# Performance work log

Measured on AMD Instinct MI355X. Metric: run time of the kernel, lower is better.

The kernel has to match this reference:

```python
import jax, jax.numpy as jnp
import numpy as np

N = 50000
E = 800000
D_IN = 128
H = 128
K = 64
BN_EPS = 1e-5


def setup_inputs() -> dict:
    key = jax.random.key(0)
    ks = jax.random.split(key, 16)
    s_in = 1.0 / np.sqrt(D_IN)
    s_h = 1.0 / np.sqrt(H)
    inp = {
        "x": jax.random.normal(ks[0], (N, D_IN), dtype=jnp.float32),
        "edge_index": jax.random.randint(ks[1], (2, E), 0, N, dtype=jnp.int64),
        # GIN layer 1 MLP (Linear(D_IN,H) -> ReLU -> Linear(H,H)), eps1, BN1
        "W1a": jax.random.uniform(ks[2], (D_IN, H), jnp.float32, -s_in, s_in),
        "b1a": jnp.zeros((H,), jnp.float32),
        "W1b": jax.random.uniform(ks[3], (H, H), jnp.float32, -s_h, s_h),
        "b1b": jnp.zeros((H,), jnp.float32),
        "eps1": jnp.zeros((), jnp.float32),
        "gamma1": jnp.ones((H,), jnp.float32),
        "beta1": jnp.zeros((H,), jnp.float32),
        # GIN layer 2 MLP, eps2, BN2
        "W2a": jax.random.uniform(ks[4], (H, H), jnp.float32, -s_h, s_h),
        "b2a": jnp.zeros((H,), jnp.float32),
        "W2b": jax.random.uniform(ks[5], (H, H), jnp.float32, -s_h, s_h),
        "b2b": jnp.zeros((H,), jnp.float32),
        "eps2": jnp.zeros((), jnp.float32),
        "gamma2": jnp.ones((H,), jnp.float32),
        "beta2": jnp.zeros((H,), jnp.float32),
        # final projection (no bias) and learnable log temperature
        "Wout": jax.random.uniform(ks[6], (H, K), jnp.float32, -s_h, s_h),
        "log_tau": jnp.zeros((), jnp.float32),  # log(1.0)
    }
    return inp


def _gin_layer(x, src, dst, Wa, ba, Wb, bb, eps):
    # GINConv: mlp((1+eps)*x + sum_{j in N(i)} x_j), scatter-add over edges
    agg = jax.ops.segment_sum(x[src], dst, num_segments=N)  # [N, d]
    h = (1.0 + eps) * x + agg
    h = jax.nn.relu(h @ Wa + ba) @ Wb + bb
    return h


def _batchnorm(x, gamma, beta):
    # training-mode BatchNorm1d over node dim (biased variance)
    m = jnp.mean(x, axis=0)
    v = jnp.mean(jnp.square(x - m), axis=0)
    return (x - m) * jax.lax.rsqrt(v + BN_EPS) * gamma + beta


def reference(x, edge_index, W1a, b1a, W1b, b1b, eps1, gamma1, beta1,
              W2a, b2a, W2b, b2b, eps2, gamma2, beta2, Wout, log_tau):
    src, dst = edge_index[0], edge_index[1]
    h = _gin_layer(x, src, dst, W1a, b1a, W1b, b1b, eps1)
    h = jax.nn.relu(_batchnorm(h, gamma1, beta1))
    h = _gin_layer(h, src, dst, W2a, b2a, W2b, b2b, eps2)
    h = jax.nn.relu(_batchnorm(h, gamma2, beta2))
    logits = h @ Wout  # [N, K]
    tau = jnp.exp(log_tau)
    S = jax.nn.softmax(logits / tau, axis=-1)
    return (S, logits)
```

## Files before the change

### kernel.cpp

```cpp
#include <hip/hip_runtime.h>
#include <hip/hip_fp16.h>


#define NNODES 50000
#define NEDGES 800000
#define HD 128
#define KOUT 64
#define NCLS 8
#define CLSW 6250
#define HIST_BLKS 512

typedef __attribute__((ext_vector_type(8))) _Float16 f16x8;
typedef __attribute__((ext_vector_type(4))) float f32x4;

__device__ __forceinline__ unsigned short f2h_bits(float f) {
    _Float16 h = (_Float16)f;
    return __builtin_bit_cast(unsigned short, h);
}
__device__ __forceinline__ f16x8 h8_relu(f16x8 v) {
    #pragma unroll
    for (int i = 0; i < 8; ++i) v[i] = (v[i] > (_Float16)0.f) ? v[i] : (_Float16)0.f;
    return v;
}

__global__ __launch_bounds__(256) void prep_all(
    const float* __restrict__ x, unsigned short* __restrict__ xh,
    const float* __restrict__ W1a, const float* __restrict__ W1b,
    const float* __restrict__ W2a, const float* __restrict__ W2b,
    unsigned short* __restrict__ wt1a, unsigned short* __restrict__ wt1b,
    unsigned short* __restrict__ wt2a, unsigned short* __restrict__ wt2b,
    const int* __restrict__ ei, int* __restrict__ deg)
{
    __shared__ int h[CLSW];
    int bid = blockIdx.x;
    if (bid < HIST_BLKS) {
        const int cls = bid & 7;
        const int lo = cls * CLSW;
        const int e0 = (bid >> 3) * 12500;
        for (int i = threadIdx.x; i < CLSW; i += 256) h[i] = 0;
        __syncthreads();
        for (int e = e0 + threadIdx.x; e < e0 + 12500; e += 256) {
            unsigned d = (unsigned)(ei[NEDGES + e] - lo);
            if (d < (unsigned)CLSW) atomicAdd(&h[d], 1);
        }
        __syncthreads();
        for (int i = threadIdx.x; i < CLSW; i += 256) {
            int v = h[i];
            if (v) atomicAdd(&deg[lo + i], v);
        }
    } else if (bid < HIST_BLKS + 6250) {
        int i = (bid - HIST_BLKS) * 256 + threadIdx.x;
        float4 v = ((const float4*)x)[i];
        ushort4 o;
        o.x = f2h_bits(v.x); o.y = f2h_bits(v.y);
        o.z = f2h_bits(v.z); o.w = f2h_bits(v.w);
        ((ushort4*)xh)[i] = o;
    } else {
        int wb = bid - (HIST_BLKS + 6250);
        int w = wb >> 6;
        int idx = (wb & 63) * 256 + threadIdx.x;
        int n = idx >> 7, k = idx & 127;
        const float* W = (w == 0) ? W1a : (w == 1) ? W1b : (w == 2) ? W2a : W2b;
        unsigned short* Wt = (w == 0) ? wt1a : (w == 1) ? wt1b : (w == 2) ? wt2a : wt2b;
        Wt[idx] = f2h_bits(W[k * HD + n]);
    }
}

__global__ __launch_bounds__(256) void scan_a(
    const int* __restrict__ deg, int* __restrict__ incl, int* __restrict__ bsum)
{
    __shared__ int s[256];
    int t = threadIdx.x, idx = blockIdx.x * 256 + t;
    int v = (idx < NNODES) ? deg[idx] : 0;
    s[t] = v; __syncthreads();
    #pragma unroll
    for (int off = 1; off < 256; off <<= 1) {
        int tmp = (t >= off) ? s[t - off] : 0;
        __syncthreads();
        s[t] += tmp;
        __syncthreads();
    }
    if (idx < NNODES) incl[idx] = s[t];
    if (t == 255) bsum[blockIdx.x] = s[255];
}

__global__ __launch_bounds__(256) void scan_b(
    const int* __restrict__ bsum, int* __restrict__ bscan, int nblk)
{
    __shared__ int s[256];
    int t = threadIdx.x;
    s[t] = (t < nblk) ? bsum[t] : 0; __syncthreads();
    #pragma unroll
    for (int off = 1; off < 256; off <<= 1) {
        int tmp = (t >= off) ? s[t - off] : 0;
        __syncthreads();
        s[t] += tmp;
        __syncthreads();
    }
    bscan[t] = s[t];
}

__global__ __launch_bounds__(256) void scan_c(
    const int* __restrict__ deg, const int* __restrict__ incl,
    const int* __restrict__ bscan,
    int* __restrict__ row_start, int* __restrict__ cur)
{
    int b = blockIdx.x, t = threadIdx.x, idx = b * 256 + t;
    if (idx >= NNODES) return;
    int off = (b > 0) ? bscan[b - 1] : 0;
    int ex = incl[idx] - deg[idx] + off;
    row_start[idx] = ex;
    cur[idx] = ex;
}

__global__ __launch_bounds__(256) void edge_fill(
    const int* __restrict__ ei, int* __restrict__ cur, int* __restrict__ col)
{
    const int cls = blockIdx.x & 7;
    const int e0 = (blockIdx.x >> 3) * 3125;
    for (int e = e0 + threadIdx.x; e < e0 + 3125; e += 256) {
        int dst = ei[NEDGES + e];
        if (dst / CLSW == cls) {
            int pos = atomicAdd(&cur[dst], 1);
            col[pos] = ei[e];
        }
    }
}

template<bool BN>
__global__ __launch_bounds__(256) void gin_gather_w(
    const unsigned short* __restrict__ Xh, const int* __restrict__ col,
    const int* __restrict__ rs, const int* __restrict__ re,
    const float* __restrict__ eps,
    const float* __restrict__ ssum, const float* __restrict__ ssq,
    const float* __restrict__ gamma, const float* __restrict__ beta,
    unsigned short* __restrict__ H0h)
{
    __shared__ float s_sc[128], s_sh[128];
    const int t = threadIdx.x;
    const int g = t >> 4;
    const int lane = t & 15;
    const f16x8* X8 = (const f16x8*)Xh;
    const float alphaf = 1.f + eps[0];

    if (BN) {
        if (t < 128) {
            const float invN = 1.0f / (float)NNODES;
            float m = ssum[t] * invN;
            float var = fmaf(-m, m, ssq[t] * invN);
            float rsq = rsqrtf(var + 1e-5f);
            float sc = gamma[t] * rsq;
            s_sc[t] = sc;
            s_sh[t] = fmaf(-m, sc, beta[t]);
        }
        __syncthreads();
    }

    f16x8 sc8, sh8, al8;
    #pragma unroll
    for (int i = 0; i < 8; ++i) al8[i] = (_Float16)alphaf;
    if (BN) {
        #pragma unroll
        for (int i = 0; i < 8; ++i) {
            sc8[i] = (_Float16)s_sc[lane * 8 + i];
            sh8[i] = (_Float16)s_sh[lane * 8 + i];
        }
    }

    #pragma unroll 1
    for (int nn = 0; nn < 2; ++nn) {
        int node = blockIdx.x * 32 + nn * 16 + g;
        if (node >= NNODES) continue;

        f16x8 acc = X8[(long)node * 16 + lane];
        if (BN) acc = h8_relu(acc * sc8 + sh8);
        acc = acc * al8;

        int j = rs[node], end = re[node];
        for (; j + 3 < end; j += 4) {
            f16x8 u0 = X8[(long)col[j]     * 16 + lane];
            f16x8 u1 = X8[(long)col[j + 1] * 16 + lane];
            f16x8 u2 = X8[(long)col[j + 2] * 16 + lane];
            f16x8 u3 = X8[(long)col[j + 3] * 16 + lane];
            if (BN) {
                u0 = h8_relu(u0 * sc8 + sh8);
                u1 = h8_relu(u1 * sc8 + sh8);
                u2 = h8_relu(u2 * sc8 + sh8);
                u3 = h8_relu(u3 * sc8 + sh8);
            }
            acc += (u0 + u1) + (u2 + u3);
        }
        for (; j < end; ++j) {
            f16x8 u = X8[(long)col[j] * 16 + lane];
            if (BN) u = h8_relu(u * sc8 + sh8);
            acc += u;
        }

        ((f16x8*)H0h)[(long)node * 16 + lane] = acc;
    }
}

__global__ __launch_bounds__(256) void mlp_mfma(
    const unsigned short* __restrict__ A,
    const unsigned short* __restrict__ Wta,
    const float* __restrict__ biasa,
    const unsigned short* __restrict__ Wtb,
    const float* __restrict__ biasb,
    unsigned short* __restrict__ Cb,
    float* __restrict__ Cf,
    float* __restrict__ out_sum, float* __restrict__ out_sq)
{
    __shared__ float4 smem4[(34816 + 17408) / 16];
    char* smem = (char*)smem4;
    _Float16 (*Wbuf)[136] = (_Float16(*)[136])smem;
    _Float16 (*Cs16)[136] = (_Float16(*)[136])(smem + 34816);
    float (*CsF)[132] = (float(*)[132])smem;
    float* redp = (float*)(smem + 34816);

    const int t = threadIdx.x;
    const int wave = t >> 6, lane = t & 63;
    const int m16 = lane & 15, quad = lane >> 4;
    const int row0 = blockIdx.x * 64;
    const int arow = row0 + wave * 16 + m16;

    float4 wreg[8];
    #pragma unroll
    for (int i = 0; i < 8; ++i) {
        int idx = t + i * 256;
        int r = idx >> 4, s = idx & 15;
        *(float4*)&Wbuf[r][s * 8] = ((const float4*)Wta)[idx];
        wreg[i] = ((const float4*)Wtb)[idx];
    }

    f16x8 afrag[4];
    if (arow < NNODES) {
        const _Float16* ar = (const _Float16*)A + (long)arow * HD + quad * 8;
        #pragma unroll
        for (int kc = 0; kc < 4; ++kc)
            afrag[kc] = *(const f16x8*)(ar + kc * 32);
    } else {
        #pragma unroll
        for (int kc = 0; kc < 4; ++kc)
            afrag[kc] = f16x8{0, 0, 0, 0, 0, 0, 0, 0};
    }
    __syncthreads();

    f32x4 accs[8];
    #pragma unroll
    for (int np = 0; np < 8; np += 2) {
        f32x4 a0 = {0.f, 0.f, 0.f, 0.f};
        f32x4 a1 = {0.f, 0.f, 0.f, 0.f};
        const _Float16* b0 = &Wbuf[np * 16 + m16][quad * 8];
        const _Float16* b1 = &Wbuf[(np + 1) * 16 + m16][quad * 8];
        #pragma unroll
        for (int kc = 0; kc < 4; ++kc) {
            f16x8 f0 = *(const f16x8*)(b0 + kc * 32);
            f16x8 f1 = *(const f16x8*)(b1 + kc * 32);
            a0 = __builtin_amdgcn_mfma_f32_16x16x32_f16(afrag[kc], f0, a0, 0, 0, 0);
            a1 = __builtin_amdgcn_mfma_f32_16x16x32_f16(afrag[kc], f1, a1, 0, 0, 0);
        }
        accs[np] = a0; accs[np + 1] = a1;
    }
    __syncthreads();

    #pragma unroll
    for (int i = 0; i < 8; ++i) {
        int idx = t + i * 256;
        int r = idx >> 4, s = idx & 15;
        *(float4*)&Wbuf[r][s * 8] = wreg[i];
    }
    #pragma unroll
    for (int np = 0; np < 8; ++np) {
        int c = np * 16 + m16;
        float bb = biasa[c];
        #pragma unroll
        for (int r = 0; r < 4; ++r)
            Cs16[wave * 16 + quad * 4 + r][c] =
                (_Float16)fmaxf(accs[np][r] + bb, 0.f);
    }
    __syncthreads();

    f16x8 afrag2[4];
    {
        const int crow = wave * 16 + m16;
        #pragma unroll
        for (int kc = 0; kc < 4; ++kc)
            afrag2[kc] = *(const f16x8*)&Cs16[crow][quad * 8 + kc * 32];
    }
    #pragma unroll
    for (int np = 0; np < 8; np += 2) {
        f32x4 a0 = {0.f, 0.f, 0.f, 0.f};
        f32x4 a1 = {0.f, 0.f, 0.f, 0.f};
        const _Float16* b0 = &Wbuf[np * 16 + m16][quad * 8];
        const _Float16* b1 = &Wbuf[(np + 1) * 16 + m16][quad * 8];
        #pragma unroll
        for (int kc = 0; kc < 4; ++kc) {
            f16x8 f0 = *(const f16x8*)(b0 + kc * 32);
            f16x8 f1 = *(const f16x8*)(b1 + kc * 32);
            a0 = __builtin_amdgcn_mfma_f32_16x16x32_f16(afrag2[kc], f0, a0, 0, 0, 0);
            a1 = __builtin_amdgcn_mfma_f32_16x16x32_f16(afrag2[kc], f1, a1, 0, 0, 0);
        }
        accs[np] = a0; accs[np + 1] = a1;
    }
    __syncthreads();

    #pragma unroll
    for (int np = 0; np < 8; ++np) {
        int c = np * 16 + m16;
        float bb = biasb[c];
        #pragma unroll
        for (int r = 0; r < 4; ++r)
            CsF[wave * 16 + quad * 4 + r][c] = accs[np][r] + bb;
    }
    __syncthreads();

    const int s4 = t & 31;
    const int rb = t >> 5;
    float lsum[4] = {}, lsq[4] = {};
    #pragma unroll
    for (int i = 0; i < 8; ++i) {
        int r = rb + i * 8;
        int row = row0 + r;
        float4 v = *(const float4*)&CsF[r][s4 * 4];
        if (row < NNODES) {
            if (Cb) {
                ushort4 o;
                o.x = f2h_bits(v.x); o.y = f2h_bits(v.y);
                o.z = f2h_bits(v.z); o.w = f2h_bits(v.w);
                ((ushort4*)Cb)[(long)row * 32 + s4] = o;
            }
            if (Cf) ((float4*)Cf)[(long)row * 32 + s4] = v;
            lsum[0] += v.x; lsum[1] += v.y; lsum[2] += v.z; lsum[3] += v.w;
            lsq[0] = fmaf(v.x, v.x, lsq[0]);
            lsq[1] = fmaf(v.y, v.y, lsq[1]);
            lsq[2] = fmaf(v.z, v.z, lsq[2]);
            lsq[3] = fmaf(v.w, v.w, lsq[3]);
        }
    }
    #pragma unroll
    for (int j = 0; j < 4; ++j) {
        redp[(0 * 8 + rb) * 128 + s4 * 4 + j] = lsum[j];
        redp[(1 * 8 + rb) * 128 + s4 * 4 + j] = lsq[j];
    }
    __syncthreads();
    if (t < 128) {
        float s = 0.f, q = 0.f;
        #pragma unroll
        for (int g = 0; g < 8; ++g) {
            s += redp[g * 128 + t];
            q += redp[(8 + g) * 128 + t];
        }
        atomicAdd(&out_sum[t], s);
        atomicAdd(&out_sq[t],  q);
    }
}

__global__ __launch_bounds__(256) void out_proj_softmax(
    const float* __restrict__ H, const float* __restrict__ Wout,
    const float* __restrict__ ssum, const float* __restrict__ ssq,
    const float* __restrict__ gamma, const float* __restrict__ beta,
    const float* __restrict__ log_tau,
    float* __restrict__ outS, float* __restrict__ outL)
{
    __shared__ float As[HD][20];
    __shared__ float s_sc[128], s_sh[128];
    const int t = threadIdx.x;
    const long row0 = (long)blockIdx.x * 16;

    if (t < 128) {
        const float invN = 1.0f / (float)NNODES;
        float m = ssum[t] * invN;
        float var = fmaf(-m, m, ssq[t] * invN);
        float rsq = rsqrtf(var + 1e-5f);
        float sc = gamma[t] * rsq;
        s_sc[t] = sc;
        s_sh[t] = fmaf(-m, sc, beta[t]);
    }
    __syncthreads();

    #pragma unroll
    for (int i = 0; i < 8; ++i) {
        int idx = t + i * 256;
        int r = idx >> 7, cc = idx & 127;
        float v = H[(row0 + r) * HD + cc];
        As[cc][r] = fmaxf(fmaf(v, s_sc[cc], s_sh[cc]), 0.f);
    }
    __syncthreads();

    const int c = t & 63;
    const int g = t >> 6;
    float acc[4] = {};

    float wq[8];
    #pragma unroll
    for (int i = 0; i < 8; ++i) wq[i] = Wout[i * KOUT + c];

    #pragma unroll 1
    for (int kc = 0; kc < HD; kc += 8) {
        float wn[8];
        if (kc + 8 < HD) {
            #pragma unroll
            for (int i = 0; i < 8; ++i) wn[i] = Wout[(kc + 8 + i) * KOUT + c];
        }
        #pragma unroll
        for (int i = 0; i < 8; ++i) {
            float4 a = *(const float4*)&As[kc + i][g * 4];
            acc[0] = fmaf(a.x, wq[i], acc[0]);
            acc[1] = fmaf(a.y, wq[i], acc[1]);
            acc[2] = fmaf(a.z, wq[i], acc[2]);
            acc[3] = fmaf(a.w, wq[i], acc[3]);
        }
        if (kc + 8 < HD) {
            #pragma unroll
            for (int i = 0; i < 8; ++i) wq[i] = wn[i];
        }
    }

    float inv_tau = __expf(-log_tau[0]);
    #pragma unroll
    for (int i = 0; i < 4; ++i) {
        float z = acc[i] * inv_tau;
        float m = z;
        #pragma unroll
        for (int o = 32; o > 0; o >>= 1) m = fmaxf(m, __shfl_xor(m, o));
        float e = __expf(z - m);
        float s = e;
        #pragma unroll
        for (int o = 32; o > 0; o >>= 1) s += __shfl_xor(s, o);
        long oi = (row0 + g * 4 + i) * KOUT + c;
        outS[oi] = e / s;
        outL[oi] = acc[i];
    }
}

extern "C" void kernel_launch(void* const* d_in, const int* in_sizes, int n_in,
                              void* d_out, int out_size, void* d_ws, size_t ws_size,
                              hipStream_t stream)
{
    const float* x      = (const float*)d_in[0];
    const int*   ei     = (const int*)d_in[1];
    const float* W1a    = (const float*)d_in[2];
    const float* b1a    = (const float*)d_in[3];
    const float* W1b    = (const float*)d_in[4];
    const float* b1b    = (const float*)d_in[5];
    const float* eps1   = (const float*)d_in[6];
    const float* gamma1 = (const float*)d_in[7];
    const float* beta1  = (const float*)d_in[8];
    const float* W2a    = (const float*)d_in[9];
    const float* b2a    = (const float*)d_in[10];
    const float* W2b    = (const float*)d_in[11];
    const float* b2b    = (const float*)d_in[12];
    const float* eps2   = (const float*)d_in[13];
    const float* gamma2 = (const float*)d_in[14];
    const float* beta2  = (const float*)d_in[15];
    const float* Wout   = (const float*)d_in[16];
    const float* ltau   = (const float*)d_in[17];

    const size_t NB = (size_t)NNODES * HD;
    float* B0 = (float*)d_ws;
    float* B1 = B0 + NB;
    float* B2 = B1 + NB;
    float* ST = B2 + NB;
    float* sum1 = ST, *sq1 = ST + 128, *sum2 = ST + 256, *sq2 = ST + 384;

    unsigned short* xh  = (unsigned short*)B2;
    unsigned short* h0h = (unsigned short*)B0;
    unsigned short* hh  = (unsigned short*)B0;
    unsigned short* h2h = (unsigned short*)B2;

    int* I0        = (int*)(ST + 1024);
    int* deg       = I0;
    int* incl      = I0 + 50048;
    int* row_start = I0 + 2 * 50048;
    int* cur       = I0 + 3 * 50048;
    int* bsum      = I0 + 4 * 50048;
    int* bscan     = bsum + 256;
    int* col       = bscan + 256;
    unsigned short* wt1a = (unsigned short*)(col + NEDGES);
    unsigned short* wt1b = wt1a + HD * HD;
    unsigned short* wt2a = wt1b + HD * HD;
    unsigned short* wt2b = wt2a + HD * HD;

    const int SCAN_BLKS = (NNODES + 255) / 256;
    const int GEMM_BLKS = (NNODES + 63) / 64;
    const int GATH_BLKS = (NNODES + 31) / 32;

    hipMemsetAsync(ST, 0, 512 * sizeof(float), stream);
    hipMemsetAsync(deg, 0, NNODES * sizeof(int), stream);
    prep_all<<<HIST_BLKS + 6506, 256, 0, stream>>>(x, xh, W1a, W1b, W2a, W2b,
                                                   wt1a, wt1b, wt2a, wt2b, ei, deg);
    scan_a<<<SCAN_BLKS, 256, 0, stream>>>(deg, incl, bsum);
    scan_b<<<1, 256, 0, stream>>>(bsum, bscan, SCAN_BLKS);
    scan_c<<<SCAN_BLKS, 256, 0, stream>>>(deg, incl, bscan, row_start, cur);
    edge_fill<<<2048, 256, 0, stream>>>(ei, cur, col);

    gin_gather_w<false><<<GATH_BLKS, 256, 0, stream>>>(
        xh, col, row_start, cur, eps1, nullptr, nullptr, nullptr, nullptr, h0h);
    mlp_mfma<<<GEMM_BLKS, 256, 0, stream>>>(
        h0h, wt1a, b1a, wt1b, b1b, hh, nullptr, sum1, sq1);

    gin_gather_w<true><<<GATH_BLKS, 256, 0, stream>>>(
        hh, col, row_start, cur, eps2, sum1, sq1, gamma1, beta1, h2h);
    mlp_mfma<<<GEMM_BLKS, 256, 0, stream>>>(
        h2h, wt2a, b2a, wt2b, b2b, nullptr, B1, sum2, sq2);

    out_proj_softmax<<<NNODES / 16, 256, 0, stream>>>(
        B1, Wout, sum2, sq2, gamma2, beta2, ltau,
        (float*)d_out, (float*)d_out + (size_t)NNODES * KOUT);
}
```

Measured before the change: 333.8 us.

## Fuse neighbor gather into the MFMA MLP kernel, reading weights from global

Merges the gather/aggregate kernel with the two-layer MLP kernel, so each 64-node block aggregates its neighbors into shared memory and feeds that tile straight into the MFMA matmuls. This removes the intermediate fp16 aggregate round trip through global memory and one launch per layer. Weight tiles are now read directly from global (L2-cached) for the MFMA B operands instead of being staged in LDS, which shrinks LDS use but adds uncached-pattern global loads in the inner loop. Gather parallelism per block changes from 32 to 64 nodes, which halves block count for the latency-bound gather phase.

```diff
diff --git a/kernel.cpp b/kernel.cpp
--- a/kernel.cpp
+++ b/kernel.cpp
@@ -128,20 +128,28 @@
 }
 
 template<bool BN>
-__global__ __launch_bounds__(256) void gin_gather_w(
+__global__ __launch_bounds__(256) void gin_gather_mlp(
     const unsigned short* __restrict__ Xh, const int* __restrict__ col,
     const int* __restrict__ rs, const int* __restrict__ re,
     const float* __restrict__ eps,
     const float* __restrict__ ssum, const float* __restrict__ ssq,
     const float* __restrict__ gamma, const float* __restrict__ beta,
-    unsigned short* __restrict__ H0h)
-{
-    __shared__ float s_sc[128], s_sh[128];
+    const unsigned short* __restrict__ Wta, const float* __restrict__ biasa,
+    const unsigned short* __restrict__ Wtb, const float* __restrict__ biasb,
+    unsigned short* __restrict__ Cb,
+    float* __restrict__ Cf,
+    float* __restrict__ out_sum, float* __restrict__ out_sq)
+{
+    __shared__ float4 smem4[(33280 + 1024) / 16];
+    char* smem = (char*)smem4;
+    _Float16 (*Ah)[136] = (_Float16(*)[136])smem;
+    float (*CsF)[130]   = (float(*)[130])smem;
+    float* redp = (float*)smem;
+    float* s_sc = (float*)(smem + 33280);
+    float* s_sh = s_sc + 128;
+
     const int t = threadIdx.x;
-    const int g = t >> 4;
-    const int lane = t & 15;
-    const f16x8* X8 = (const f16x8*)Xh;
-    const float alphaf = 1.f + eps[0];
+    const int row0 = blockIdx.x * 64;
 
     if (BN) {
         if (t < 128) {
@@ -156,102 +164,74 @@
         __syncthreads();
     }
 
-    f16x8 sc8, sh8, al8;
-    #pragma unroll
-    for (int i = 0; i < 8; ++i) al8[i] = (_Float16)alphaf;
-    if (BN) {
-        #pragma unroll
-        for (int i = 0; i < 8; ++i) {
-            sc8[i] = (_Float16)s_sc[lane * 8 + i];
-            sh8[i] = (_Float16)s_sh[lane * 8 + i];
-        }
-    }
-
-    #pragma unroll 1
-    for (int nn = 0; nn < 2; ++nn) {
-        int node = blockIdx.x * 32 + nn * 16 + g;
-        if (node >= NNODES) continue;
-
-        f16x8 acc = X8[(long)node * 16 + lane];
-        if (BN) acc = h8_relu(acc * sc8 + sh8);
-        acc = acc * al8;
-
-        int j = rs[node], end = re[node];
-        for (; j + 3 < end; j += 4) {
-            f16x8 u0 = X8[(long)col[j]     * 16 + lane];
-            f16x8 u1 = X8[(long)col[j + 1] * 16 + lane];
-            f16x8 u2 = X8[(long)col[j + 2] * 16 + lane];
-            f16x8 u3 = X8[(long)col[j + 3] * 16 + lane];
-            if (BN) {
-                u0 = h8_relu(u0 * sc8 + sh8);
-                u1 = h8_relu(u1 * sc8 + sh8);
-                u2 = h8_relu(u2 * sc8 + sh8);
-                u3 = h8_relu(u3 * sc8 + sh8);
+    {
+        const int g = t >> 4;
+        const int lane = t & 15;
+        const f16x8* X8 = (const f16x8*)Xh;
+        const float alphaf = 1.f + eps[0];
+
+        f16x8 sc8, sh8, al8;
+        #pragma unroll
+        for (int i = 0; i < 8; ++i) al8[i] = (_Float16)alphaf;
+        if (BN) {
+            #pragma unroll
+            for (int i = 0; i < 8; ++i) {
+                sc8[i] = (_Float16)s_sc[lane * 8 + i];
+                sh8[i] = (_Float16)s_sh[lane * 8 + i];
             }
-            acc += (u0 + u1) + (u2 + u3);
-        }
-        for (; j < end; ++j) {
-            f16x8 u = X8[(long)col[j] * 16 + lane];
-            if (BN) u = h8_relu(u * sc8 + sh8);
-            acc += u;
-        }
-
-        ((f16x8*)H0h)[(long)node * 16 + lane] = acc;
-    }
-}
-
-__global__ __launch_bounds__(256) void mlp_mfma(
-    const unsigned short* __restrict__ A,
-    const unsigned short* __restrict__ Wta,
-    const float* __restrict__ biasa,
-    const unsigned short* __restrict__ Wtb,
-    const float* __restrict__ biasb,
-    unsigned short* __restrict__ Cb,
-    float* __restrict__ Cf,
-    float* __restrict__ out_sum, float* __restrict__ out_sq)
-{
-    __shared__ float4 smem4[(34816 + 17408) / 16];
-    char* smem = (char*)smem4;
-    _Float16 (*Wbuf)[136] = (_Float16(*)[136])smem;
-    _Float16 (*Cs16)[136] = (_Float16(*)[136])(smem + 34816);
-    float (*CsF)[132] = (float(*)[132])smem;
-    float* redp = (float*)(smem + 34816);
-
-    const int t = threadIdx.x;
-    const int wave = t >> 6, lane = t & 63;
-    const int m16 = lane & 15, quad = lane >> 4;
-    const int row0 = blockIdx.x * 64;
-    const int arow = row0 + wave * 16 + m16;
-
-    float4 wreg[8];
-    #pragma unroll
-    for (int i = 0; i < 8; ++i) {
-        int idx = t + i * 256;
-        int r = idx >> 4, s = idx & 15;
-        *(float4*)&Wbuf[r][s * 8] = ((const float4*)Wta)[idx];
-        wreg[i] = ((const float4*)Wtb)[idx];
-    }
+        }
+
+        #pragma unroll 1
+        for (int nn = 0; nn < 4; ++nn) {
+            int local = nn * 16 + g;
+            int node = row0 + local;
+            f16x8 acc = f16x8{0, 0, 0, 0, 0, 0, 0, 0};
+            if (node < NNODES) {
+                acc = X8[(long)node * 16 + lane];
+                if (BN) acc = h8_relu(acc * sc8 + sh8);
+                acc = acc * al8;
+                int j = rs[node], end = re[node];
+                for (; j + 3 < end; j += 4) {
+                    f16x8 u0 = X8[(long)col[j]     * 16 + lane];
+                    f16x8 u1 = X8[(long)col[j + 1] * 16 + lane];
+                    f16x8 u2 = X8[(long)col[j + 2] * 16 + lane];
+                    f16x8 u3 = X8[(long)col[j + 3] * 16 + lane];
+                    if (BN) {
+                        u0 = h8_relu(u0 * sc8 + sh8);
+                        u1 = h8_relu(u1 * sc8 + sh8);
+                        u2 = h8_relu(u2 * sc8 + sh8);
+                        u3 = h8_relu(u3 * sc8 + sh8);
+                    }
+                    acc += (u0 + u1) + (u2 + u3);
+                }
+                for (; j < end; ++j) {
+                    f16x8 u = X8[(long)col[j] * 16 + lane];
+                    if (BN) u = h8_relu(u * sc8 + sh8);
+                    acc += u;
+                }
+            }
+            *(f16x8*)&Ah[local][lane * 8] = acc;
+        }
+    }
+    __syncthreads();
+
+    const int wave = t >> 6, lane64 = t & 63;
+    const int m16 = lane64 & 15, quad = lane64 >> 4;
+    const _Float16* WtaH = (const _Float16*)Wta;
+    const _Float16* WtbH = (const _Float16*)Wtb;
 
     f16x8 afrag[4];
-    if (arow < NNODES) {
-        const _Float16* ar = (const _Float16*)A + (long)arow * HD + quad * 8;
-        #pragma unroll
-        for (int kc = 0; kc < 4; ++kc)
-            afrag[kc] = *(const f16x8*)(ar + kc * 32);
-    } else {
-        #pragma unroll
-        for (int kc = 0; kc < 4; ++kc)
-            afrag[kc] = f16x8{0, 0, 0, 0, 0, 0, 0, 0};
-    }
-    __syncthreads();
+    #pragma unroll
+    for (int kc = 0; kc < 4; ++kc)
+        afrag[kc] = *(const f16x8*)&Ah[wave * 16 + m16][quad * 8 + kc * 32];
 
     f32x4 accs[8];
     #pragma unroll
     for (int np = 0; np < 8; np += 2) {
         f32x4 a0 = {0.f, 0.f, 0.f, 0.f};
         f32x4 a1 = {0.f, 0.f, 0.f, 0.f};
-        const _Float16* b0 = &Wbuf[np * 16 + m16][quad * 8];
-        const _Float16* b1 = &Wbuf[(np + 1) * 16 + m16][quad * 8];
+        const _Float16* b0 = WtaH + (np * 16 + m16) * HD + quad * 8;
+        const _Float16* b1 = WtaH + ((np + 1) * 16 + m16) * HD + quad * 8;
         #pragma unroll
         for (int kc = 0; kc < 4; ++kc) {
             f16x8 f0 = *(const f16x8*)(b0 + kc * 32);
@@ -261,38 +241,29 @@
         }
         accs[np] = a0; accs[np + 1] = a1;
     }
-    __syncthreads();
-
-    #pragma unroll
-    for (int i = 0; i < 8; ++i) {
-        int idx = t + i * 256;
-        int r = idx >> 4, s = idx & 15;
-        *(float4*)&Wbuf[r][s * 8] = wreg[i];
-    }
+
     #pragma unroll
     for (int np = 0; np < 8; ++np) {
         int c = np * 16 + m16;
         float bb = biasa[c];
         #pragma unroll
         for (int r = 0; r < 4; ++r)
-            Cs16[wave * 16 + quad * 4 + r][c] =
+            Ah[wave * 16 + quad * 4 + r][c] =
                 (_Float16)fmaxf(accs[np][r] + bb, 0.f);
     }
     __syncthreads();
 
     f16x8 afrag2[4];
-    {
-        const int crow = wave * 16 + m16;
-        #pragma unroll
-        for (int kc = 0; kc < 4; ++kc)
-            afrag2[kc] = *(const f16x8*)&Cs16[crow][quad * 8 + kc * 32];
-    }
+    #pragma unroll
+    for (int kc = 0; kc < 4; ++kc)
+        afrag2[kc] = *(const f16x8*)&Ah[wave * 16 + m16][quad * 8 + kc * 32];
+
     #pragma unroll
     for (int np = 0; np < 8; np += 2) {
         f32x4 a0 = {0.f, 0.f, 0.f, 0.f};
         f32x4 a1 = {0.f, 0.f, 0.f, 0.f};
-        const _Float16* b0 = &Wbuf[np * 16 + m16][quad * 8];
-        const _Float16* b1 = &Wbuf[(np + 1) * 16 + m16][quad * 8];
+        const _Float16* b0 = WtbH + (np * 16 + m16) * HD + quad * 8;
+        const _Float16* b1 = WtbH + ((np + 1) * 16 + m16) * HD + quad * 8;
         #pragma unroll
         for (int kc = 0; kc < 4; ++kc) {
             f16x8 f0 = *(const f16x8*)(b0 + kc * 32);
@@ -337,6 +308,8 @@
             lsq[3] = fmaf(v.w, v.w, lsq[3]);
         }
     }
+    __syncthreads();
+
     #pragma unroll
     for (int j = 0; j < 4; ++j) {
         redp[(0 * 8 + rb) * 128 + s4 * 4 + j] = lsum[j];
@@ -346,9 +319,9 @@
     if (t < 128) {
         float s = 0.f, q = 0.f;
         #pragma unroll
-        for (int g = 0; g < 8; ++g) {
-            s += redp[g * 128 + t];
-            q += redp[(8 + g) * 128 + t];
+        for (int g2 = 0; g2 < 8; ++g2) {
+            s += redp[g2 * 128 + t];
+            q += redp[(8 + g2) * 128 + t];
         }
         atomicAdd(&out_sum[t], s);
         atomicAdd(&out_sq[t],  q);
@@ -464,9 +437,7 @@
     float* sum1 = ST, *sq1 = ST + 128, *sum2 = ST + 256, *sq2 = ST + 384;
 
     unsigned short* xh  = (unsigned short*)B2;
-    unsigned short* h0h = (unsigned short*)B0;
     unsigned short* hh  = (unsigned short*)B0;
-    unsigned short* h2h = (unsigned short*)B2;
 
     int* I0        = (int*)(ST + 1024);
     int* deg       = I0;
@@ -483,7 +454,6 @@
 
     const int SCAN_BLKS = (NNODES + 255) / 256;
     const int GEMM_BLKS = (NNODES + 63) / 64;
-    const int GATH_BLKS = (NNODES + 31) / 32;
 
     hipMemsetAsync(ST, 0, 512 * sizeof(float), stream);
     hipMemsetAsync(deg, 0, NNODES * sizeof(int), stream);
@@ -494,15 +464,15 @@
     scan_c<<<SCAN_BLKS, 256, 0, stream>>>(deg, incl, bscan, row_start, cur);
     edge_fill<<<2048, 256, 0, stream>>>(ei, cur, col);
 
-    gin_gather_w<false><<<GATH_BLKS, 256, 0, stream>>>(
-        xh, col, row_start, cur, eps1, nullptr, nullptr, nullptr, nullptr, h0h);
-    mlp_mfma<<<GEMM_BLKS, 256, 0, stream>>>(
-        h0h, wt1a, b1a, wt1b, b1b, hh, nullptr, sum1, sq1);
-
-    gin_gather_w<true><<<GATH_BLKS, 256, 0, stream>>>(
-        hh, col, row_start, cur, eps2, sum1, sq1, gamma1, beta1, h2h);
-    mlp_mfma<<<GEMM_BLKS, 256, 0, stream>>>(
-        h2h, wt2a, b2a, wt2b, b2b, nullptr, B1, sum2, sq2);
+    gin_gather_mlp<false><<<GEMM_BLKS, 256, 0, stream>>>(
+        xh, col, row_start, cur, eps1,
+        nullptr, nullptr, nullptr, nullptr,
+        wt1a, b1a, wt1b, b1b, hh, nullptr, sum1, sq1);
+
+    gin_gather_mlp<true><<<GEMM_BLKS, 256, 0, stream>>>(
+        hh, col, row_start, cur, eps2,
+        sum1, sq1, gamma1, beta1,
+        wt2a, b2a, wt2b, b2b, nullptr, B1, sum2, sq2);
 
     out_proj_softmax<<<NNODES / 16, 256, 0, stream>>>(
         B1, Wout, sum2, sq2, gamma2, beta2, ltau,
```

After: 343.3 us. 1.03x slower.
